# Kernel optimization log

Measured on AMD Instinct MI355X. Metric: run time of the kernel, lower is better.

## Reference

```python
import jax, jax.numpy as jnp
import numpy as np

GROUP_SIZE = 128
QMAX = 127.0  # int8 symmetric: 2^(8-1) - 1
EPS = 1e-8


def group_quant_dequant(t, group_size=GROUP_SIZE):
    """Group-wise symmetric int8 fake-quantize along the last dim.

    Groups of `group_size` along the last axis share one scale
    s = max|t| / 127; values are rounded/clipped to int8 range and
    immediately dequantized (q * s), which is the exact math of a
    group-quantized GEMM with inline dequantization.
    """
    shape = t.shape
    g = t.reshape(shape[:-1] + (shape[-1] // group_size, group_size))
    s = jnp.maximum(jnp.max(jnp.abs(g), axis=-1, keepdims=True) / QMAX, EPS)
    q = jnp.clip(jnp.round(g / s), -QMAX, QMAX)
    return (q * s).reshape(shape)


def setup_inputs() -> dict:
    key = jax.random.key(0)
    k0, k1, k2, k3 = jax.random.split(key, 4)
    B, S, H, I = 2, 2048, 4096, 11008
    x = jax.random.normal(k0, (B, S, H), dtype=jnp.float32)
    # Linear weights stored [out_features, in_features]; quant groups run
    # along the in_features (contraction) axis.
    w_gate = jax.random.normal(k1, (I, H), dtype=jnp.float32) * (1.0 / np.sqrt(H))
    w_up = jax.random.normal(k2, (I, H), dtype=jnp.float32) * (1.0 / np.sqrt(H))
    w_down = jax.random.normal(k3, (H, I), dtype=jnp.float32) * (1.0 / np.sqrt(I))
    return {"x": x, "w_gate": w_gate, "w_up": w_up, "w_down": w_down}


def reference(x, w_gate, w_up, w_down):
    # quantize input activations (QuantTensor(x))
    xq = group_quant_dequant(x)
    # gate/up quant-GEMMs with inline weight dequant
    gate = jnp.einsum('bsh,ih->bsi', xq, group_quant_dequant(w_gate))
    up = jnp.einsum('bsh,ih->bsi', xq, group_quant_dequant(w_up))
    # SwiGLU: SiLU(gate) * up, then requantize the hidden activation
    hidden = jax.nn.silu(gate) * up
    hq = group_quant_dequant(hidden)
    # down quant-GEMM -> dequantized float output
    out = jnp.einsum('bsi,hi->bsh', hq, group_quant_dequant(w_down))
    return out
```

## Files before the change

kernel.cpp:

```cpp
#include <hip/hip_runtime.h>
#include <math.h>

typedef int i32x4 __attribute__((ext_vector_type(4)));
typedef float f32x4 __attribute__((ext_vector_type(4)));
typedef float f32x2 __attribute__((ext_vector_type(2)));

#define QMAXF 127.0f
#define EPSQ 1e-8f

__device__ __forceinline__ void gl_lds16(const void* g, void* l) {
  __builtin_amdgcn_global_load_lds(
      (const __attribute__((address_space(1))) unsigned int*)g,
      (__attribute__((address_space(3))) unsigned int*)l, 16, 0, 0);
}
__device__ __forceinline__ void gl_lds4(const void* g, void* l) {
  __builtin_amdgcn_global_load_lds(
      (const __attribute__((address_space(1))) unsigned int*)g,
      (__attribute__((address_space(3))) unsigned int*)l, 4, 0, 0);
}

__global__ __launch_bounds__(256)
void qdq8(const float* __restrict__ in, char* __restrict__ q,
          float* __restrict__ sT, long n_groups, int gpr, int R) {
  long wid = (long)blockIdx.x * 4 + (threadIdx.x >> 6);
  if (wid >= n_groups) return;
  int lane = threadIdx.x & 63;
  long base = wid * 128 + lane * 2;
  f32x2 v = *(const f32x2*)(in + base);
  float m = fmaxf(fabsf(v.x), fabsf(v.y));
#pragma unroll
  for (int off = 32; off; off >>= 1) m = fmaxf(m, __shfl_xor(m, off));
  float s = fmaxf(m / QMAXF, EPSQ);
  int q0 = (int)fminf(fmaxf(rintf(v.x / s), -QMAXF), QMAXF);
  int q1 = (int)fminf(fmaxf(rintf(v.y / s), -QMAXF), QMAXF);
  *(unsigned short*)(q + base) =
      (unsigned short)((q0 & 0xff) | ((q1 & 0xff) << 8));
  if (lane == 0) {
    long row = wid / gpr;
    long gc = wid - row * gpr;
    sT[gc * (long)R + row] = s;
  }
}


#define GU_SC 131072
#define GU_RMX 135168
#define GU_RS 137216
#define GU_LDS 138240

__global__ __launch_bounds__(512, 2)
void gemm_gu_i8(const char* __restrict__ Aq, const char* __restrict__ Bg,
                const char* __restrict__ Bu,
                const float* __restrict__ sAT, const float* __restrict__ sGT,
                const float* __restrict__ sUT,
                char* __restrict__ Hq, float* __restrict__ sHT,
                int M, int N, int K, int NBN) {
  extern __shared__ __align__(16) char smem[];
  const int tid = threadIdx.x;
  const int lane = tid & 63;
  const int wid = tid >> 6;
  const int wm = wid >> 1, wn = wid & 1;
  const int wr = wm * 64, wc = wn * 64;
  const int l15 = lane & 15, l16 = lane >> 4;

  const int nwg = gridDim.x;
  const int wg = ((int)blockIdx.x & 7) * (nwg >> 3) + ((int)blockIdx.x >> 3);
  const long m0 = (long)(wg / NBN) * 256;
  const long n0 = (long)(wg % NBN) * 128;

  const long rowS = tid >> 3;
  const int offS = ((tid & 7) * 16) ^ ((int)(rowS & 7) << 4);
  const long kstr = 64L * K;
  const char* gA0 = Aq + (m0 + rowS) * K + offS;
  const char* gG0 = Bg + (n0 + rowS) * K + offS;
  const char* gU0 = Bu + (n0 + rowS) * K + offS;

  const int rdSwz = (l15 & 7) << 4;
  const int colK0 = (l16 * 16) ^ rdSwz;
  const int colK1 = (64 + l16 * 16) ^ rdSwz;

  f32x4 accg[4][4], accu[4][4];
#pragma unroll
  for (int i = 0; i < 4; i++)
#pragma unroll
    for (int j = 0; j < 4; j++) {
      accg[i][j] = (f32x4){0.f, 0.f, 0.f, 0.f};
      accu[i][j] = (f32x4){0.f, 0.f, 0.f, 0.f};
    }
  const i32x4 iz = {0, 0, 0, 0};
  const int KG = K >> 7;

#define GU_STAGE(gg, bb)                                                      \
  {                                                                           \
    const long kb = (long)(gg) << 7;                                          \
    char* tb = smem + (bb) * 65536;                                           \
    _Pragma("unroll") for (int k = 0; k < 4; k++)                             \
        gl_lds16(gA0 + kb + k * kstr, tb + (tid + 512 * k) * 16);             \
    _Pragma("unroll") for (int k = 0; k < 2; k++) {                           \
      gl_lds16(gG0 + kb + k * kstr, tb + 32768 + (tid + 512 * k) * 16);       \
      gl_lds16(gU0 + kb + k * kstr, tb + 49152 + (tid + 512 * k) * 16);       \
    }                                                                         \
    char* sc = smem + GU_SC + (bb) * 2048;                                    \
    if (wid < 4) {                                                            \
      gl_lds4(sAT + (long)(gg) * M + m0 + tid, sc + wid * 256);               \
    } else if (wid < 6) {                                                     \
      gl_lds4(sGT + (long)(gg) * N + n0 + (tid - 256), sc + 1024 + (wid - 4) * 256); \
    } else {                                                                  \
      gl_lds4(sUT + (long)(gg) * N + n0 + (tid - 384), sc + 1536 + (wid - 6) * 256); \
    }                                                                         \
  }

  GU_STAGE(0, 0);
  __syncthreads();

  for (int g = 0; g < KG; ++g) {
    const int cb = g & 1;
    if (g + 1 < KG) GU_STAGE(g + 1, cb ^ 1);

    const char* tb = smem + cb * 65536;
    const float* sc = (const float*)(smem + GU_SC + cb * 2048);

    i32x4 af[4][2];
#pragma unroll
    for (int i = 0; i < 4; i++) {
      const int rb = (wr + i * 16 + l15) * 128;
      af[i][0] = *(const i32x4*)(tb + rb + colK0);
      af[i][1] = *(const i32x4*)(tb + rb + colK1);
    }
    f32x4 sa4[4];
#pragma unroll
    for (int i = 0; i < 4; i++)
      sa4[i] = *(const f32x4*)(sc + wr + i * 16 + l16 * 4);

#pragma unroll
    for (int j = 0; j < 4; j++) {
      const int rbB = (wc + j * 16 + l15) * 128;
      i32x4 bgf[2], buf_[2];
      bgf[0] = *(const i32x4*)(tb + 32768 + rbB + colK0);
      bgf[1] = *(const i32x4*)(tb + 32768 + rbB + colK1);
      buf_[0] = *(const i32x4*)(tb + 49152 + rbB + colK0);
      buf_[1] = *(const i32x4*)(tb + 49152 + rbB + colK1);
      float sbg = sc[256 + wc + j * 16 + l15];
      float sbu = sc[384 + wc + j * 16 + l15];
#pragma unroll
      for (int i = 0; i < 4; i++) {
        i32x4 tg = __builtin_amdgcn_mfma_i32_16x16x64_i8(af[i][0], bgf[0], iz, 0, 0, 0);
        tg = __builtin_amdgcn_mfma_i32_16x16x64_i8(af[i][1], bgf[1], tg, 0, 0, 0);
        i32x4 tu = __builtin_amdgcn_mfma_i32_16x16x64_i8(af[i][0], buf_[0], iz, 0, 0, 0);
        tu = __builtin_amdgcn_mfma_i32_16x16x64_i8(af[i][1], buf_[1], tu, 0, 0, 0);
        f32x4 mg = sa4[i] * sbg;
        f32x4 mu = sa4[i] * sbu;
        accg[i][j] += mg * __builtin_convertvector(tg, f32x4);
        accu[i][j] += mu * __builtin_convertvector(tu, f32x4);
      }
    }
    __syncthreads();
  }

  float* rmx = (float*)(smem + GU_RMX);
  float* rs = (float*)(smem + GU_RS);
  float pm[4][4];
#pragma unroll
  for (int i = 0; i < 4; i++)
#pragma unroll
    for (int r = 0; r < 4; r++) pm[i][r] = 0.f;
#pragma unroll
  for (int i = 0; i < 4; i++)
#pragma unroll
    for (int j = 0; j < 4; j++)
#pragma unroll
      for (int r = 0; r < 4; r++) {
        float gv = accg[i][j][r];
        float h = gv / (1.f + expf(-gv)) * accu[i][j][r];
        accu[i][j][r] = h;
        pm[i][r] = fmaxf(pm[i][r], fabsf(h));
      }
#pragma unroll
  for (int i = 0; i < 4; i++)
#pragma unroll
    for (int r = 0; r < 4; r++) {
      pm[i][r] = fmaxf(pm[i][r], __shfl_xor(pm[i][r], 1));
      pm[i][r] = fmaxf(pm[i][r], __shfl_xor(pm[i][r], 2));
      pm[i][r] = fmaxf(pm[i][r], __shfl_xor(pm[i][r], 4));
      pm[i][r] = fmaxf(pm[i][r], __shfl_xor(pm[i][r], 8));
    }
#pragma unroll
  for (int i = 0; i < 4; i++)
#pragma unroll
    for (int r = 0; r < 4; r++)
      if (l15 == i * 4 + r) rmx[wn * 256 + wr + i * 16 + l16 * 4 + r] = pm[i][r];
  __syncthreads();
  if (tid < 256) {
    float mx = fmaxf(rmx[tid], rmx[256 + tid]);
    float s = fmaxf(mx / QMAXF, EPSQ);
    rs[tid] = s;
    sHT[(n0 >> 7) * (long)M + m0 + tid] = s;
  }
  __syncthreads();
  char* sQ = smem;
#pragma unroll
  for (int i = 0; i < 4; i++) {
    f32x4 sr = *(const f32x4*)(rs + wr + i * 16 + l16 * 4);
#pragma unroll
    for (int j = 0; j < 4; j++)
#pragma unroll
      for (int r = 0; r < 4; r++) {
        float qv = fminf(fmaxf(rintf(accu[i][j][r] / sr[r]), -QMAXF), QMAXF);
        sQ[(wr + i * 16 + l16 * 4 + r) * 128 + wc + j * 16 + l15] = (char)(int)qv;
      }
  }
  __syncthreads();
  {
    int row = tid >> 1, seg = tid & 1;
    const i32x4* src = (const i32x4*)(sQ + row * 128 + seg * 64);
    i32x4* dst = (i32x4*)(Hq + (m0 + row) * N + n0 + seg * 64);
#pragma unroll
    for (int k = 0; k < 4; k++) dst[k] = src[k];
  }
}

#define DN_SC 98304
#define DN_LDS 101376

__global__ __launch_bounds__(512, 2)
void gemm_dn_i8(const char* __restrict__ Aq, const char* __restrict__ Bq,
                const float* __restrict__ sAT, const float* __restrict__ sBT,
                float* __restrict__ C, int M, int N, int K, int NBN) {
  extern __shared__ __align__(16) char smem[];
  const int tid = threadIdx.x;
  const int lane = tid & 63;
  const int wid = tid >> 6;
  const int wm = wid >> 1, wn = wid & 1;
  const int wr = wm * 64, wc = wn * 64;
  const int l15 = lane & 15, l16 = lane >> 4;

  const int nwg = gridDim.x;
  const int wg = ((int)blockIdx.x & 7) * (nwg >> 3) + ((int)blockIdx.x >> 3);
  const long m0 = (long)(wg / NBN) * 256;
  const long n0 = (long)(wg % NBN) * 128;

  const long rowS = tid >> 3;
  const int offS = ((tid & 7) * 16) ^ ((int)(rowS & 7) << 4);
  const long kstr = 64L * K;
  const char* gA0 = Aq + (m0 + rowS) * K + offS;
  const char* gB0 = Bq + (n0 + rowS) * K + offS;

  const int rdSwz = (l15 & 7) << 4;
  const int colK0 = (l16 * 16) ^ rdSwz;
  const int colK1 = (64 + l16 * 16) ^ rdSwz;

  f32x4 acc[4][4];
#pragma unroll
  for (int i = 0; i < 4; i++)
#pragma unroll
    for (int j = 0; j < 4; j++) acc[i][j] = (f32x4){0.f, 0.f, 0.f, 0.f};
  const i32x4 iz = {0, 0, 0, 0};
  const int KG = K >> 7;

#define DN_STAGE(gg, bb)                                                      \
  {                                                                           \
    const long kb = (long)(gg) << 7;                                          \
    char* tb = smem + (bb) * 49152;                                           \
    _Pragma("unroll") for (int k = 0; k < 4; k++)                             \
        gl_lds16(gA0 + kb + k * kstr, tb + (tid + 512 * k) * 16);             \
    _Pragma("unroll") for (int k = 0; k < 2; k++)                             \
        gl_lds16(gB0 + kb + k * kstr, tb + 32768 + (tid + 512 * k) * 16);     \
    char* sc = smem + DN_SC + (bb) * 1536;                                    \
    if (wid < 4) {                                                            \
      gl_lds4(sAT + (long)(gg) * M + m0 + tid, sc + wid * 256);               \
    } else if (wid < 6) {                                                     \
      gl_lds4(sBT + (long)(gg) * N + n0 + (tid - 256), sc + 1024 + (wid - 4) * 256); \
    }                                                                         \
  }

  DN_STAGE(0, 0);
  __syncthreads();

  for (int g = 0; g < KG; ++g) {
    const int cb = g & 1;
    if (g + 1 < KG) DN_STAGE(g + 1, cb ^ 1);

    const char* tb = smem + cb * 49152;
    const float* sc = (const float*)(smem + DN_SC + cb * 1536);

    i32x4 af[4][2];
#pragma unroll
    for (int i = 0; i < 4; i++) {
      const int rb = (wr + i * 16 + l15) * 128;
      af[i][0] = *(const i32x4*)(tb + rb + colK0);
      af[i][1] = *(const i32x4*)(tb + rb + colK1);
    }
    f32x4 sa4[4];
#pragma unroll
    for (int i = 0; i < 4; i++)
      sa4[i] = *(const f32x4*)(sc + wr + i * 16 + l16 * 4);

#pragma unroll
    for (int j = 0; j < 4; j++) {
      const int rbB = (wc + j * 16 + l15) * 128;
      i32x4 bf[2];
      bf[0] = *(const i32x4*)(tb + 32768 + rbB + colK0);
      bf[1] = *(const i32x4*)(tb + 32768 + rbB + colK1);
      float sb = sc[256 + wc + j * 16 + l15];
#pragma unroll
      for (int i = 0; i < 4; i++) {
        i32x4 t = __builtin_amdgcn_mfma_i32_16x16x64_i8(af[i][0], bf[0], iz, 0, 0, 0);
        t = __builtin_amdgcn_mfma_i32_16x16x64_i8(af[i][1], bf[1], t, 0, 0, 0);
        f32x4 ms = sa4[i] * sb;
        acc[i][j] += ms * __builtin_convertvector(t, f32x4);
      }
    }
    __syncthreads();
  }

#pragma unroll
  for (int i = 0; i < 4; i++)
#pragma unroll
    for (int j = 0; j < 4; j++)
#pragma unroll
      for (int r = 0; r < 4; r++) {
        long row = m0 + wr + i * 16 + l16 * 4 + r;
        long col = n0 + wc + j * 16 + l15;
        C[row * N + col] = acc[i][j][r];
      }
}

extern "C" void kernel_launch(void* const* d_in, const int* in_sizes, int n_in,
                              void* d_out, int out_size, void* d_ws, size_t ws_size,
                              hipStream_t stream) {
  (void)n_in; (void)out_size;
  const float* x  = (const float*)d_in[0];
  const float* wg = (const float*)d_in[1];
  const float* wu = (const float*)d_in[2];
  const float* wd = (const float*)d_in[3];
  float* out = (float*)d_out;

  const long H = 4096;
  const long M = in_sizes[0] / H;
  const long I = in_sizes[1] / H;
  const long GH = H >> 7;
  const long GI = I >> 7;

  char* ws = (char*)d_ws;
  size_t off = 0;
  char* xq  = ws + off; off += (size_t)(M * H);
  char* wgq = ws + off; off += (size_t)(I * H);
  char* wuq = ws + off; off += (size_t)(I * H);
  char* wdq = ws + off; off += (size_t)(H * I);
  char* hq  = ws + off; off += (size_t)(M * I);
  float* s_x = (float*)(ws + off); off += (size_t)(GH * M) * 4;
  float* s_g = (float*)(ws + off); off += (size_t)(GH * I) * 4;
  float* s_u = (float*)(ws + off); off += (size_t)(GH * I) * 4;
  float* s_d = (float*)(ws + off); off += (size_t)(GI * H) * 4;
  float* s_h = (float*)(ws + off); off += (size_t)(GI * M) * 4;
  if (ws_size < off) return;

  hipFuncSetAttribute((const void*)gemm_gu_i8,
                      hipFuncAttributeMaxDynamicSharedMemorySize, GU_LDS);
  hipFuncSetAttribute((const void*)gemm_dn_i8,
                      hipFuncAttributeMaxDynamicSharedMemorySize, DN_LDS);

  {
    long ng;
    ng = M * H / 128;
    qdq8<<<dim3((unsigned)((ng + 3) / 4)), dim3(256), 0, stream>>>(x, xq, s_x, ng, (int)GH, (int)M);
    ng = I * H / 128;
    qdq8<<<dim3((unsigned)((ng + 3) / 4)), dim3(256), 0, stream>>>(wg, wgq, s_g, ng, (int)GH, (int)I);
    qdq8<<<dim3((unsigned)((ng + 3) / 4)), dim3(256), 0, stream>>>(wu, wuq, s_u, ng, (int)GH, (int)I);
    ng = H * I / 128;
    qdq8<<<dim3((unsigned)((ng + 3) / 4)), dim3(256), 0, stream>>>(wd, wdq, s_d, ng, (int)GI, (int)H);
  }

  {
    const int NBN = (int)GI;
    const int grid = (int)(M / 256) * NBN;
    gemm_gu_i8<<<dim3(grid), dim3(512), GU_LDS, stream>>>(
        xq, wgq, wuq, s_x, s_g, s_u, hq, s_h, (int)M, (int)I, (int)H, NBN);
  }
  {
    const int NBN = (int)GH;
    const int grid = (int)(M / 256) * NBN;
    gemm_dn_i8<<<dim3(grid), dim3(512), DN_LDS, stream>>>(
        hq, wdq, s_h, s_d, out, (int)M, (int)H, (int)I, NBN);
  }
}
```

Baseline: 1.117 ms.

## Split gate/up across 16 waves with 1024-thread blocks and LDS exchange

The gate/up GEMM moves to 1024-thread blocks that cover a 128x128 tile. Waves 0-7 compute gate and waves 8-15 compute up, and gate results pass through LDS to the up waves for the SiLU, requantisation and row-max steps. The down GEMM also moves to 1024 threads, with 16 waves each owning a 64x32 sub-tile of the same 256x128 tile. The aim is lower per-wave register pressure and more resident waves to hide latency, at the cost of an extra LDS round trip and barrier in the epilogue and a smaller M tile in gate/up, which lowers A/B reuse.

Result: no change. 1.135 ms (+1.6%).

```diff
diff --git a/kernel.cpp b/kernel.cpp
--- a/kernel.cpp
+++ b/kernel.cpp
@@ -43,12 +43,12 @@
 }
 
 
-#define GU_SC 131072
-#define GU_RMX 135168
-#define GU_RS 137216
-#define GU_LDS 138240
-
-__global__ __launch_bounds__(512, 2)
+#define GU_SC 98304
+#define GU_RMX 101376
+#define GU_RS 103424
+#define GU_LDS 103936
+
+__global__ __launch_bounds__(1024, 4)
 void gemm_gu_i8(const char* __restrict__ Aq, const char* __restrict__ Bg,
                 const char* __restrict__ Bu,
                 const float* __restrict__ sAT, const float* __restrict__ sGT,
@@ -59,18 +59,19 @@
   const int tid = threadIdx.x;
   const int lane = tid & 63;
   const int wid = tid >> 6;
-  const int wm = wid >> 1, wn = wid & 1;
-  const int wr = wm * 64, wc = wn * 64;
+  const int w8 = wid & 7;
+  const bool is_up = wid >= 8;
+  const int wr = (w8 >> 2) * 64;
+  const int wc = (w8 & 3) * 32;
   const int l15 = lane & 15, l16 = lane >> 4;
 
   const int nwg = gridDim.x;
   const int wg = ((int)blockIdx.x & 7) * (nwg >> 3) + ((int)blockIdx.x >> 3);
-  const long m0 = (long)(wg / NBN) * 256;
+  const long m0 = (long)(wg / NBN) * 128;
   const long n0 = (long)(wg % NBN) * 128;
 
   const long rowS = tid >> 3;
   const int offS = ((tid & 7) * 16) ^ ((int)(rowS & 7) << 4);
-  const long kstr = 64L * K;
   const char* gA0 = Aq + (m0 + rowS) * K + offS;
   const char* gG0 = Bg + (n0 + rowS) * K + offS;
   const char* gU0 = Bu + (n0 + rowS) * K + offS;
@@ -79,35 +80,28 @@
   const int colK0 = (l16 * 16) ^ rdSwz;
   const int colK1 = (64 + l16 * 16) ^ rdSwz;
 
-  f32x4 accg[4][4], accu[4][4];
+  f32x4 acc[4][2];
 #pragma unroll
   for (int i = 0; i < 4; i++)
 #pragma unroll
-    for (int j = 0; j < 4; j++) {
-      accg[i][j] = (f32x4){0.f, 0.f, 0.f, 0.f};
-      accu[i][j] = (f32x4){0.f, 0.f, 0.f, 0.f};
-    }
+    for (int j = 0; j < 2; j++) acc[i][j] = (f32x4){0.f, 0.f, 0.f, 0.f};
   const i32x4 iz = {0, 0, 0, 0};
   const int KG = K >> 7;
 
 #define GU_STAGE(gg, bb)                                                      \
   {                                                                           \
     const long kb = (long)(gg) << 7;                                          \
-    char* tb = smem + (bb) * 65536;                                           \
-    _Pragma("unroll") for (int k = 0; k < 4; k++)                             \
-        gl_lds16(gA0 + kb + k * kstr, tb + (tid + 512 * k) * 16);             \
-    _Pragma("unroll") for (int k = 0; k < 2; k++) {                           \
-      gl_lds16(gG0 + kb + k * kstr, tb + 32768 + (tid + 512 * k) * 16);       \
-      gl_lds16(gU0 + kb + k * kstr, tb + 49152 + (tid + 512 * k) * 16);       \
-    }                                                                         \
-    char* sc = smem + GU_SC + (bb) * 2048;                                    \
-    if (wid < 4) {                                                            \
-      gl_lds4(sAT + (long)(gg) * M + m0 + tid, sc + wid * 256);               \
-    } else if (wid < 6) {                                                     \
-      gl_lds4(sGT + (long)(gg) * N + n0 + (tid - 256), sc + 1024 + (wid - 4) * 256); \
-    } else {                                                                  \
-      gl_lds4(sUT + (long)(gg) * N + n0 + (tid - 384), sc + 1536 + (wid - 6) * 256); \
-    }                                                                         \
+    char* tb = smem + (bb) * 49152;                                           \
+    gl_lds16(gA0 + kb, tb + tid * 16);                                        \
+    gl_lds16(gG0 + kb, tb + 16384 + tid * 16);                                \
+    gl_lds16(gU0 + kb, tb + 32768 + tid * 16);                                \
+    char* sc = smem + GU_SC + (bb) * 1536;                                    \
+    if (wid == 0)      gl_lds4(sAT + (long)(gg) * M + m0 + lane,      sc);        \
+    else if (wid == 1) gl_lds4(sAT + (long)(gg) * M + m0 + 64 + lane, sc + 256);  \
+    else if (wid == 2) gl_lds4(sGT + (long)(gg) * N + n0 + lane,      sc + 512);  \
+    else if (wid == 3) gl_lds4(sGT + (long)(gg) * N + n0 + 64 + lane, sc + 768);  \
+    else if (wid == 4) gl_lds4(sUT + (long)(gg) * N + n0 + lane,      sc + 1024); \
+    else if (wid == 5) gl_lds4(sUT + (long)(gg) * N + n0 + 64 + lane, sc + 1280); \
   }
 
   GU_STAGE(0, 0);
@@ -117,8 +111,9 @@
     const int cb = g & 1;
     if (g + 1 < KG) GU_STAGE(g + 1, cb ^ 1);
 
-    const char* tb = smem + cb * 65536;
-    const float* sc = (const float*)(smem + GU_SC + cb * 2048);
+    const char* tb = smem + cb * 49152;
+    const char* tbB = tb + (is_up ? 32768 : 16384);
+    const float* scp = (const float*)(smem + GU_SC + cb * 1536);
 
     i32x4 af[4][2];
 #pragma unroll
@@ -130,99 +125,107 @@
     f32x4 sa4[4];
 #pragma unroll
     for (int i = 0; i < 4; i++)
-      sa4[i] = *(const f32x4*)(sc + wr + i * 16 + l16 * 4);
-
-#pragma unroll
-    for (int j = 0; j < 4; j++) {
+      sa4[i] = *(const f32x4*)(scp + wr + i * 16 + l16 * 4);
+    const int sbBase = is_up ? 256 : 128;
+#pragma unroll
+    for (int j = 0; j < 2; j++) {
       const int rbB = (wc + j * 16 + l15) * 128;
-      i32x4 bgf[2], buf_[2];
-      bgf[0] = *(const i32x4*)(tb + 32768 + rbB + colK0);
-      bgf[1] = *(const i32x4*)(tb + 32768 + rbB + colK1);
-      buf_[0] = *(const i32x4*)(tb + 49152 + rbB + colK0);
-      buf_[1] = *(const i32x4*)(tb + 49152 + rbB + colK1);
-      float sbg = sc[256 + wc + j * 16 + l15];
-      float sbu = sc[384 + wc + j * 16 + l15];
+      i32x4 bf0 = *(const i32x4*)(tbB + rbB + colK0);
+      i32x4 bf1 = *(const i32x4*)(tbB + rbB + colK1);
+      float sb = scp[sbBase + wc + j * 16 + l15];
 #pragma unroll
       for (int i = 0; i < 4; i++) {
-        i32x4 tg = __builtin_amdgcn_mfma_i32_16x16x64_i8(af[i][0], bgf[0], iz, 0, 0, 0);
-        tg = __builtin_amdgcn_mfma_i32_16x16x64_i8(af[i][1], bgf[1], tg, 0, 0, 0);
-        i32x4 tu = __builtin_amdgcn_mfma_i32_16x16x64_i8(af[i][0], buf_[0], iz, 0, 0, 0);
-        tu = __builtin_amdgcn_mfma_i32_16x16x64_i8(af[i][1], buf_[1], tu, 0, 0, 0);
-        f32x4 mg = sa4[i] * sbg;
-        f32x4 mu = sa4[i] * sbu;
-        accg[i][j] += mg * __builtin_convertvector(tg, f32x4);
-        accu[i][j] += mu * __builtin_convertvector(tu, f32x4);
+        i32x4 t = __builtin_amdgcn_mfma_i32_16x16x64_i8(af[i][0], bf0, iz, 0, 0, 0);
+        t = __builtin_amdgcn_mfma_i32_16x16x64_i8(af[i][1], bf1, t, 0, 0, 0);
+        acc[i][j] += (sa4[i] * sb) * __builtin_convertvector(t, f32x4);
       }
     }
     __syncthreads();
   }
 
+  float* gexch = (float*)smem;
+  if (!is_up) {
+#pragma unroll
+    for (int i = 0; i < 4; i++)
+#pragma unroll
+      for (int j = 0; j < 2; j++)
+#pragma unroll
+        for (int r = 0; r < 4; r++)
+          gexch[(wr + i * 16 + l16 * 4 + r) * 128 + wc + j * 16 + l15] = acc[i][j][r];
+  }
+  __syncthreads();
   float* rmx = (float*)(smem + GU_RMX);
   float* rs = (float*)(smem + GU_RS);
-  float pm[4][4];
-#pragma unroll
-  for (int i = 0; i < 4; i++)
-#pragma unroll
-    for (int r = 0; r < 4; r++) pm[i][r] = 0.f;
-#pragma unroll
-  for (int i = 0; i < 4; i++)
-#pragma unroll
-    for (int j = 0; j < 4; j++)
+  if (is_up) {
+    float pm[4][4];
+#pragma unroll
+    for (int i = 0; i < 4; i++)
+#pragma unroll
+      for (int r = 0; r < 4; r++) pm[i][r] = 0.f;
+#pragma unroll
+    for (int i = 0; i < 4; i++)
+#pragma unroll
+      for (int j = 0; j < 2; j++)
+#pragma unroll
+        for (int r = 0; r < 4; r++) {
+          int row = wr + i * 16 + l16 * 4 + r;
+          int col = wc + j * 16 + l15;
+          float gv = gexch[row * 128 + col];
+          float h = gv / (1.f + expf(-gv)) * acc[i][j][r];
+          acc[i][j][r] = h;
+          pm[i][r] = fmaxf(pm[i][r], fabsf(h));
+        }
+#pragma unroll
+    for (int i = 0; i < 4; i++)
 #pragma unroll
       for (int r = 0; r < 4; r++) {
-        float gv = accg[i][j][r];
-        float h = gv / (1.f + expf(-gv)) * accu[i][j][r];
-        accu[i][j][r] = h;
-        pm[i][r] = fmaxf(pm[i][r], fabsf(h));
+        pm[i][r] = fmaxf(pm[i][r], __shfl_xor(pm[i][r], 1));
+        pm[i][r] = fmaxf(pm[i][r], __shfl_xor(pm[i][r], 2));
+        pm[i][r] = fmaxf(pm[i][r], __shfl_xor(pm[i][r], 4));
+        pm[i][r] = fmaxf(pm[i][r], __shfl_xor(pm[i][r], 8));
       }
 #pragma unroll
-  for (int i = 0; i < 4; i++)
-#pragma unroll
-    for (int r = 0; r < 4; r++) {
-      pm[i][r] = fmaxf(pm[i][r], __shfl_xor(pm[i][r], 1));
-      pm[i][r] = fmaxf(pm[i][r], __shfl_xor(pm[i][r], 2));
-      pm[i][r] = fmaxf(pm[i][r], __shfl_xor(pm[i][r], 4));
-      pm[i][r] = fmaxf(pm[i][r], __shfl_xor(pm[i][r], 8));
-    }
-#pragma unroll
-  for (int i = 0; i < 4; i++)
-#pragma unroll
-    for (int r = 0; r < 4; r++)
-      if (l15 == i * 4 + r) rmx[wn * 256 + wr + i * 16 + l16 * 4 + r] = pm[i][r];
-  __syncthreads();
-  if (tid < 256) {
-    float mx = fmaxf(rmx[tid], rmx[256 + tid]);
+    for (int i = 0; i < 4; i++)
+#pragma unroll
+      for (int r = 0; r < 4; r++)
+        if (l15 == i * 4 + r)
+          rmx[(w8 & 3) * 128 + wr + i * 16 + l16 * 4 + r] = pm[i][r];
+  }
+  __syncthreads();
+  if (tid < 128) {
+    float mx = fmaxf(fmaxf(rmx[tid], rmx[128 + tid]),
+                     fmaxf(rmx[256 + tid], rmx[384 + tid]));
     float s = fmaxf(mx / QMAXF, EPSQ);
     rs[tid] = s;
     sHT[(n0 >> 7) * (long)M + m0 + tid] = s;
   }
   __syncthreads();
-  char* sQ = smem;
-#pragma unroll
-  for (int i = 0; i < 4; i++) {
-    f32x4 sr = *(const f32x4*)(rs + wr + i * 16 + l16 * 4);
-#pragma unroll
-    for (int j = 0; j < 4; j++)
-#pragma unroll
-      for (int r = 0; r < 4; r++) {
-        float qv = fminf(fmaxf(rintf(accu[i][j][r] / sr[r]), -QMAXF), QMAXF);
-        sQ[(wr + i * 16 + l16 * 4 + r) * 128 + wc + j * 16 + l15] = (char)(int)qv;
-      }
+  char* qb = smem;
+  if (is_up) {
+#pragma unroll
+    for (int i = 0; i < 4; i++) {
+      f32x4 sr = *(const f32x4*)(rs + wr + i * 16 + l16 * 4);
+#pragma unroll
+      for (int j = 0; j < 2; j++)
+#pragma unroll
+        for (int r = 0; r < 4; r++) {
+          float qv = fminf(fmaxf(rintf(acc[i][j][r] / sr[r]), -QMAXF), QMAXF);
+          qb[(wr + i * 16 + l16 * 4 + r) * 128 + wc + j * 16 + l15] = (char)(int)qv;
+        }
+    }
   }
   __syncthreads();
   {
-    int row = tid >> 1, seg = tid & 1;
-    const i32x4* src = (const i32x4*)(sQ + row * 128 + seg * 64);
-    i32x4* dst = (i32x4*)(Hq + (m0 + row) * N + n0 + seg * 64);
-#pragma unroll
-    for (int k = 0; k < 4; k++) dst[k] = src[k];
+    long row = tid >> 3;
+    int off = (tid & 7) * 16;
+    *(i32x4*)(Hq + (m0 + row) * N + n0 + off) = *(const i32x4*)(qb + row * 128 + off);
   }
 }
 
 #define DN_SC 98304
 #define DN_LDS 101376
 
-__global__ __launch_bounds__(512, 2)
+__global__ __launch_bounds__(1024, 4)
 void gemm_dn_i8(const char* __restrict__ Aq, const char* __restrict__ Bq,
                 const float* __restrict__ sAT, const float* __restrict__ sBT,
                 float* __restrict__ C, int M, int N, int K, int NBN) {
@@ -230,8 +233,8 @@
   const int tid = threadIdx.x;
   const int lane = tid & 63;
   const int wid = tid >> 6;
-  const int wm = wid >> 1, wn = wid & 1;
-  const int wr = wm * 64, wc = wn * 64;
+  const int wr = (wid >> 2) * 64;
+  const int wc = (wid & 3) * 32;
   const int l15 = lane & 15, l16 = lane >> 4;
 
   const int nwg = gridDim.x;
@@ -241,19 +244,19 @@
 
   const long rowS = tid >> 3;
   const int offS = ((tid & 7) * 16) ^ ((int)(rowS & 7) << 4);
-  const long kstr = 64L * K;
   const char* gA0 = Aq + (m0 + rowS) * K + offS;
+  const char* gA1 = gA0 + 128L * K;
   const char* gB0 = Bq + (n0 + rowS) * K + offS;
 
   const int rdSwz = (l15 & 7) << 4;
   const int colK0 = (l16 * 16) ^ rdSwz;
   const int colK1 = (64 + l16 * 16) ^ rdSwz;
 
-  f32x4 acc[4][4];
+  f32x4 acc[4][2];
 #pragma unroll
   for (int i = 0; i < 4; i++)
 #pragma unroll
-    for (int j = 0; j < 4; j++) acc[i][j] = (f32x4){0.f, 0.f, 0.f, 0.f};
+    for (int j = 0; j < 2; j++) acc[i][j] = (f32x4){0.f, 0.f, 0.f, 0.f};
   const i32x4 iz = {0, 0, 0, 0};
   const int KG = K >> 7;
 
@@ -261,16 +264,16 @@
   {                                                                           \
     const long kb = (long)(gg) << 7;                                          \
     char* tb = smem + (bb) * 49152;                                           \
-    _Pragma("unroll") for (int k = 0; k < 4; k++)                             \
-        gl_lds16(gA0 + kb + k * kstr, tb + (tid + 512 * k) * 16);             \
-    _Pragma("unroll") for (int k = 0; k < 2; k++)                             \
-        gl_lds16(gB0 + kb + k * kstr, tb + 32768 + (tid + 512 * k) * 16);     \
+    gl_lds16(gA0 + kb, tb + tid * 16);                                        \
+    gl_lds16(gA1 + kb, tb + 16384 + tid * 16);                                \
+    gl_lds16(gB0 + kb, tb + 32768 + tid * 16);                                \
     char* sc = smem + DN_SC + (bb) * 1536;                                    \
-    if (wid < 4) {                                                            \
-      gl_lds4(sAT + (long)(gg) * M + m0 + tid, sc + wid * 256);               \
-    } else if (wid < 6) {                                                     \
-      gl_lds4(sBT + (long)(gg) * N + n0 + (tid - 256), sc + 1024 + (wid - 4) * 256); \
-    }                                                                         \
+    if (wid == 0)      gl_lds4(sAT + (long)(gg) * M + m0 + lane,       sc);        \
+    else if (wid == 1) gl_lds4(sAT + (long)(gg) * M + m0 + 64 + lane,  sc + 256);  \
+    else if (wid == 2) gl_lds4(sAT + (long)(gg) * M + m0 + 128 + lane, sc + 512);  \
+    else if (wid == 3) gl_lds4(sAT + (long)(gg) * M + m0 + 192 + lane, sc + 768);  \
+    else if (wid == 4) gl_lds4(sBT + (long)(gg) * N + n0 + lane,       sc + 1024); \
+    else if (wid == 5) gl_lds4(sBT + (long)(gg) * N + n0 + 64 + lane,  sc + 1280); \
   }
 
   DN_STAGE(0, 0);
@@ -281,7 +284,7 @@
     if (g + 1 < KG) DN_STAGE(g + 1, cb ^ 1);
 
     const char* tb = smem + cb * 49152;
-    const float* sc = (const float*)(smem + DN_SC + cb * 1536);
+    const float* scp = (const float*)(smem + DN_SC + cb * 1536);
 
     i32x4 af[4][2];
 #pragma unroll
@@ -293,21 +296,18 @@
     f32x4 sa4[4];
 #pragma unroll
     for (int i = 0; i < 4; i++)
-      sa4[i] = *(const f32x4*)(sc + wr + i * 16 + l16 * 4);
-
-#pragma unroll
-    for (int j = 0; j < 4; j++) {
+      sa4[i] = *(const f32x4*)(scp + wr + i * 16 + l16 * 4);
+#pragma unroll
+    for (int j = 0; j < 2; j++) {
       const int rbB = (wc + j * 16 + l15) * 128;
-      i32x4 bf[2];
-      bf[0] = *(const i32x4*)(tb + 32768 + rbB + colK0);
-      bf[1] = *(const i32x4*)(tb + 32768 + rbB + colK1);
-      float sb = sc[256 + wc + j * 16 + l15];
+      i32x4 bf0 = *(const i32x4*)(tb + 32768 + rbB + colK0);
+      i32x4 bf1 = *(const i32x4*)(tb + 32768 + rbB + colK1);
+      float sb = scp[256 + wc + j * 16 + l15];
 #pragma unroll
       for (int i = 0; i < 4; i++) {
-        i32x4 t = __builtin_amdgcn_mfma_i32_16x16x64_i8(af[i][0], bf[0], iz, 0, 0, 0);
-        t = __builtin_amdgcn_mfma_i32_16x16x64_i8(af[i][1], bf[1], t, 0, 0, 0);
-        f32x4 ms = sa4[i] * sb;
-        acc[i][j] += ms * __builtin_convertvector(t, f32x4);
+        i32x4 t = __builtin_amdgcn_mfma_i32_16x16x64_i8(af[i][0], bf0, iz, 0, 0, 0);
+        t = __builtin_amdgcn_mfma_i32_16x16x64_i8(af[i][1], bf1, t, 0, 0, 0);
+        acc[i][j] += (sa4[i] * sb) * __builtin_convertvector(t, f32x4);
       }
     }
     __syncthreads();
@@ -316,7 +316,7 @@
 #pragma unroll
   for (int i = 0; i < 4; i++)
 #pragma unroll
-    for (int j = 0; j < 4; j++)
+    for (int j = 0; j < 2; j++)
 #pragma unroll
       for (int r = 0; r < 4; r++) {
         long row = m0 + wr + i * 16 + l16 * 4 + r;
@@ -373,14 +373,14 @@
 
   {
     const int NBN = (int)GI;
-    const int grid = (int)(M / 256) * NBN;
-    gemm_gu_i8<<<dim3(grid), dim3(512), GU_LDS, stream>>>(
+    const int grid = (int)(M / 128) * NBN;
+    gemm_gu_i8<<<dim3(grid), dim3(1024), GU_LDS, stream>>>(
         xq, wgq, wuq, s_x, s_g, s_u, hq, s_h, (int)M, (int)I, (int)H, NBN);
   }
   {
     const int NBN = (int)GH;
     const int grid = (int)(M / 256) * NBN;
-    gemm_dn_i8<<<dim3(grid), dim3(512), DN_LDS, stream>>>(
+    gemm_dn_i8<<<dim3(grid), dim3(1024), DN_LDS, stream>>>(
         hq, wdq, s_h, s_d, out, (int)M, (int)H, (int)I, NBN);
   }
 }
```
